# Performance work log

Measured on AMD Instinct MI355X. Metric: run time of the kernel, lower is better.

Reference implementation:

```python
import jax, jax.numpy as jnp
import numpy as np
from jax import lax

D_MODEL, D_STATE, D_CONV, EXPAND = 1024, 16, 4, 2
D_INNER = D_MODEL * EXPAND
LN_EPS = 1e-5


def _silu(v):
    return v * jax.nn.sigmoid(v)


def setup_inputs() -> dict:
    key = jax.random.key(0)
    ks = jax.random.split(key, 12)
    B, T = 4, 2048
    x = jax.random.normal(ks[0], (B, T, D_MODEL), dtype=jnp.float32)
    W_in = jax.random.normal(ks[1], (2 * D_INNER, D_MODEL), dtype=jnp.float32) * (D_MODEL ** -0.5)
    conv_w = jax.random.normal(ks[2], (D_INNER, 1, D_CONV), dtype=jnp.float32) * (D_CONV ** -0.5)
    conv_b = jax.random.normal(ks[3], (D_INNER,), dtype=jnp.float32) * 0.01
    W_x = jax.random.normal(ks[4], (2 * D_STATE, D_INNER), dtype=jnp.float32) * (D_INNER ** -0.5)
    dt_init_std = D_INNER ** -0.5
    W_dt = jax.random.uniform(ks[5], (D_INNER, D_INNER), minval=-dt_init_std, maxval=dt_init_std, dtype=jnp.float32)
    # bias = inverse softplus of dt sampled log-uniform in [dt_min, dt_max]
    dt = jnp.exp(jax.random.uniform(ks[6], (D_INNER,)) * (np.log(0.1) - np.log(0.001)) + np.log(0.001))
    b_dt = dt + jnp.log(-jnp.expm1(-dt))
    A_log = jnp.log(jnp.arange(1, D_STATE + 1, dtype=jnp.float32) * 0.5)
    D_param = jnp.ones((D_INNER,), dtype=jnp.float32)
    W_out = jax.random.normal(ks[7], (D_MODEL, D_INNER), dtype=jnp.float32) * (D_MODEL ** -0.5)
    ln_g = jnp.ones((D_INNER,), dtype=jnp.float32)
    ln_b = jnp.zeros((D_INNER,), dtype=jnp.float32)
    return {"x": x, "W_in": W_in, "conv_w": conv_w, "conv_b": conv_b, "W_x": W_x,
            "W_dt": W_dt, "b_dt": b_dt, "A_log": A_log, "D_param": D_param,
            "W_out": W_out, "ln_g": ln_g, "ln_b": ln_b}


def _forward(x, W_in, conv_w, conv_b, W_x, W_dt, b_dt, A_log, D_param, W_out, ln_g, ln_b):
    B, T, _ = x.shape
    xz = jnp.einsum('btd,ed->bte', x, W_in)            # (B,T,2*d_inner)
    xp, z = xz[..., :D_INNER], xz[..., D_INNER:]
    # depthwise causal conv1d (left pad d_conv-1, keep first T outputs)
    xc = lax.conv_general_dilated(
        jnp.transpose(xp, (0, 2, 1)), conv_w,
        window_strides=(1,), padding=[(D_CONV - 1, 0)],
        feature_group_count=D_INNER,
        dimension_numbers=('NCH', 'OIH', 'NCH')) + conv_b[None, :, None]
    xc = _silu(jnp.transpose(xc, (0, 2, 1)))           # (B,T,d_inner)
    ssm = jnp.einsum('bti,si->bts', xc, W_x)           # (B,T,2*d_state)
    Bp, Cp = ssm[..., :D_STATE], ssm[..., D_STATE:]
    dt = jax.nn.softplus(jnp.einsum('bti,oi->bto', xc, W_dt) + b_dt)
    A = -jnp.exp(A_log)                                # (d_state,)

    def step(h, inp):
        x_t, b_t, c_t, dt_t = inp                      # (B,d),(B,s),(B,s),(B,d)
        dA = jnp.exp(dt_t[..., None] * A)              # (B,d_inner,d_state)
        h = dA * h + (dt_t[..., None] * b_t[:, None, :]) * x_t[..., None]
        y_t = jnp.einsum('bds,bs->bd', h, c_t)
        return h, y_t

    h0 = jnp.zeros((B, D_INNER, D_STATE), dtype=x.dtype)
    tm = lambda a: jnp.moveaxis(a, 1, 0)               # time-major
    _, ys = lax.scan(step, h0, (tm(xc), tm(Bp), tm(Cp), tm(dt)))
    y = jnp.moveaxis(ys, 0, 1)                         # (B,T,d_inner)

    mu = jnp.mean(y, axis=-1, keepdims=True)
    var = jnp.mean((y - mu) ** 2, axis=-1, keepdims=True)
    y = (y - mu) * lax.rsqrt(var + LN_EPS) * ln_g + ln_b
    y = y + xc * D_param
    y = y * _silu(z)
    return jnp.einsum('bti,di->btd', y, W_out)         # dropout is identity (eval)


def reference(x, W_in, conv_w, conv_b, W_x, W_dt, b_dt, A_log, D_param, W_out, ln_g, ln_b):
    return _forward(x, W_in, conv_w, conv_b, W_x, W_dt, b_dt, A_log, D_param, W_out, ln_g, ln_b)
```

## Files before the change

kernel.cpp:

```cpp
#include <hip/hip_runtime.h>
#include <hip/hip_bf16.h>
#include <math.h>
#include <stdint.h>

#define B_SZ 4
#define T_SZ 2048
#define DM   1024
#define DI   2048
#define DS   16
#define BT   (B_SZ*T_SZ)
#define NC   2176

typedef __attribute__((ext_vector_type(8))) short short8;
typedef __attribute__((ext_vector_type(4))) float f32x4;

__device__ __forceinline__ float siluf(float v) { return v / (1.f + __expf(-v)); }
__device__ __forceinline__ float softplusf(float x) {
    return fmaxf(x, 0.f) + log1pf(__expf(-fabsf(x)));
}
__device__ __forceinline__ unsigned short f2b(float f) {
    __hip_bfloat16 h = __float2bfloat16(f);
    return *reinterpret_cast<unsigned short*>(&h);
}
__device__ __forceinline__ float b2f(unsigned short u) {
    unsigned v = (unsigned)u << 16;
    float f;
    __builtin_memcpy(&f, &v, 4);
    return f;
}
__device__ __forceinline__ void gld_lds16(const void* g, void* l) {
    __builtin_amdgcn_global_load_lds(
        (const __attribute__((address_space(1))) unsigned int*)g,
        (__attribute__((address_space(3))) unsigned int*)l,
        16, 0, 0);
}

__global__ __launch_bounds__(256)
void cvt_bf16(const float* __restrict__ src, unsigned short* __restrict__ dst, int n4)
{
    int i = blockIdx.x * 256 + threadIdx.x;
    if (i >= n4) return;
    float4 v = ((const float4*)src)[i];
    ushort4 o;
    o.x = f2b(v.x); o.y = f2b(v.y); o.z = f2b(v.z); o.w = f2b(v.w);
    ((ushort4*)dst)[i] = o;
}

__global__ __launch_bounds__(256)
void cvt_wc(const float* __restrict__ Wdt, const float* __restrict__ Wx,
            unsigned short* __restrict__ dst)
{
    const int n4 = NC * (DI / 4);
    int i = blockIdx.x * 256 + threadIdx.x;
    if (i >= n4) return;
    int row = i >> 9;
    int c4  = i & 511;
    float4 v;
    if (row < 2048)      v = ((const float4*)Wdt)[(size_t)row * 512 + c4];
    else if (row < 2080) v = ((const float4*)Wx)[(size_t)(row - 2048) * 512 + c4];
    else                 v = make_float4(0.f, 0.f, 0.f, 0.f);
    ushort4 o;
    o.x = f2b(v.x); o.y = f2b(v.y); o.z = f2b(v.z); o.w = f2b(v.w);
    ((ushort4*)dst)[i] = o;
}

__global__ __launch_bounds__(512)
void gemm_mfma(const unsigned short* __restrict__ A,
               const unsigned short* __restrict__ Bm,
               int M, int N, int K, int mode,
               const float* __restrict__ bias,
               void* __restrict__ o0, void* __restrict__ o1, void* __restrict__ o2)
{
    __shared__ unsigned short As[2][128 * 32];
    __shared__ unsigned short Bs[2][128 * 32];

    const int npn = N >> 7;
    const int pid = blockIdx.x;
    const int gsz = 16 * npn;
    const int gid = pid / gsz;
    const int pm  = gid * 16 + (pid % 16);
    const int pn  = (pid % gsz) / 16;
    const int bm  = pm * 128;
    const int bn  = pn * 128;

    const int tid  = threadIdx.x;
    const int lane = tid & 63;
    const int wave = tid >> 6;
    const int wm   = (wave >> 2) * 64;
    const int wn   = (wave & 3) * 32;

    f32x4 zero4 = {0.f, 0.f, 0.f, 0.f};
    f32x4 acc[4][2];
#pragma unroll
    for (int i = 0; i < 4; i++)
#pragma unroll
        for (int j = 0; j < 2; j++) acc[i][j] = zero4;

    const int sr    = tid >> 2;
    const int sgran = (tid & 3) ^ ((tid >> 3) & 3);
    const unsigned short* Ag = A  + (size_t)(bm + sr) * K + sgran * 8;
    const unsigned short* Bg = Bm + (size_t)(bn + sr) * K + sgran * 8;

    const int fr = lane & 15;
    const int fg = lane >> 4;
    int aoff[4], boff[2];
#pragma unroll
    for (int i = 0; i < 4; i++) {
        const int l = (wm + i * 16 + fr) * 64 + fg * 16;
        aoff[i] = l ^ (((l >> 7) & 3) << 4);
    }
#pragma unroll
    for (int j = 0; j < 2; j++) {
        const int l = (wn + j * 16 + fr) * 64 + fg * 16;
        boff[j] = l ^ (((l >> 7) & 3) << 4);
    }

    gld_lds16(Ag, &As[0][tid * 8]);
    gld_lds16(Bg, &Bs[0][tid * 8]);
    __syncthreads();

    int cur = 0;
    for (int k0 = 0; k0 < K; k0 += 32) {
        if (k0 + 32 < K) {
            gld_lds16(Ag + k0 + 32, &As[cur ^ 1][tid * 8]);
            gld_lds16(Bg + k0 + 32, &Bs[cur ^ 1][tid * 8]);
        }
        const char* Ab = (const char*)&As[cur][0];
        const char* Bb = (const char*)&Bs[cur][0];
        short8 af[4], bf[2];
#pragma unroll
        for (int i = 0; i < 4; i++)
            af[i] = *(const short8*)(Ab + aoff[i]);
#pragma unroll
        for (int j = 0; j < 2; j++)
            bf[j] = *(const short8*)(Bb + boff[j]);
#pragma unroll
        for (int i = 0; i < 4; i++)
#pragma unroll
            for (int j = 0; j < 2; j++)
                acc[i][j] = __builtin_amdgcn_mfma_f32_16x16x32_bf16(
                    af[i], bf[j], acc[i][j], 0, 0, 0);
        __syncthreads();
        cur ^= 1;
    }

    const int cr0 = bm + wm + (lane >> 4) * 4;
    const int cc0 = bn + wn + (lane & 15);
#pragma unroll
    for (int i = 0; i < 4; i++) {
#pragma unroll
        for (int j = 0; j < 2; j++) {
            const int col = cc0 + j * 16;
#pragma unroll
            for (int r = 0; r < 4; r++) {
                const int row = cr0 + i * 16 + r;
                float v = acc[i][j][r];
                if (mode == 0) {
                    if (col < 2048)
                        ((unsigned short*)o0)[(size_t)row * 2048 + col] = f2b(v);
                    else
                        ((unsigned short*)o1)[(size_t)row * 2048 + col - 2048] = f2b(v);
                } else if (mode == 1) {
                    if (col < 2048) {
                        ((float*)o0)[(size_t)row * 2048 + col] = softplusf(v + bias[col]);
                    } else if (col < 2064) {
                        ((float*)o1)[(size_t)row * DS + (col - 2048)] = v;
                    } else if (col < 2080) {
                        ((float*)o2)[(size_t)row * DS + (col - 2064)] = v;
                    }
                } else {
                    ((float*)o0)[(size_t)row * N + col] = v;
                }
            }
        }
    }
}

__global__ __launch_bounds__(256)
void conv_silu(const unsigned short* __restrict__ xpb, const float* __restrict__ cw,
               const float* __restrict__ cb, unsigned short* __restrict__ xcb)
{
    const int idx = blockIdx.x * 256 + threadIdx.x;
    const int i  = idx & (DI - 1);
    const int bt = idx >> 11;
    const int t  = bt & (T_SZ - 1);
    float acc = cb[i];
    float4 w = *(const float4*)(cw + (size_t)i * 4);
    float wr[4] = {w.x, w.y, w.z, w.w};
#pragma unroll
    for (int k = 0; k < 4; k++) {
        const int tt = t - 3 + k;
        if (tt >= 0)
            acc = fmaf(b2f(xpb[(size_t)(bt - 3 + k) * DI + i]), wr[k], acc);
    }
    xcb[idx] = f2b(siluf(acc));
}

#define CH 16
#define CL (T_SZ / CH)

__global__ __launch_bounds__(256)
void scan2(const unsigned short* __restrict__ xcb, float* __restrict__ dty,
           const float* __restrict__ Bp, const float* __restrict__ Cp,
           const float* __restrict__ A_log)
{
    __shared__ float shH[CH][16][DS];
    __shared__ float shP[CH][16][DS];
    __shared__ float shI[CH][16][DS];
    const int tid = threadIdx.x;
    const int c = tid >> 4;
    const int g = tid & 15;
    const int b = blockIdx.y;
    const int d = blockIdx.x * 16 + g;

    float A[DS];
#pragma unroll
    for (int s = 0; s < DS; s++) A[s] = -__expf(A_log[s]);

    const size_t colbase = (size_t)b * T_SZ * DI + d;
    const unsigned short* xp = xcb + colbase + (size_t)c * CL * DI;
    float* dp = dty + colbase + (size_t)c * CL * DI;
    const float4* Bb = (const float4*)(Bp + ((size_t)b * T_SZ + c * CL) * DS);
    const float4* Cb = (const float4*)(Cp + ((size_t)b * T_SZ + c * CL) * DS);

    float h[DS], P[DS];
#pragma unroll
    for (int s = 0; s < DS; s++) { h[s] = 0.f; P[s] = 1.f; }

    for (int i = 0; i < CL; i++) {
        const float xv = b2f(xp[(size_t)i * DI]);
        const float dv = dp[(size_t)i * DI];
        float4 Bv[4] = {Bb[i*4+0], Bb[i*4+1], Bb[i*4+2], Bb[i*4+3]};
        const float* bs = (const float*)&Bv[0];
        const float dx = dv * xv;
#pragma unroll
        for (int s = 0; s < DS; s++) {
            const float dA = __expf(dv * A[s]);
            h[s] = fmaf(dA, h[s], dx * bs[s]);
            P[s] *= dA;
        }
    }
#pragma unroll
    for (int s = 0; s < DS; s += 4) {
        *(float4*)&shH[c][g][s] = make_float4(h[s], h[s+1], h[s+2], h[s+3]);
        *(float4*)&shP[c][g][s] = make_float4(P[s], P[s+1], P[s+2], P[s+3]);
    }
    __syncthreads();

    {
        const int g2 = tid >> 4, s2 = tid & 15;
        float hin = 0.f;
        shI[0][g2][s2] = 0.f;
        for (int cc = 1; cc < CH; cc++) {
            hin = fmaf(shP[cc-1][g2][s2], hin, shH[cc-1][g2][s2]);
            shI[cc][g2][s2] = hin;
        }
    }
    __syncthreads();

#pragma unroll
    for (int s = 0; s < DS; s++) h[s] = shI[c][g][s];
    for (int i = 0; i < CL; i++) {
        const float xv = b2f(xp[(size_t)i * DI]);
        const float dv = dp[(size_t)i * DI];
        float4 Bv[4] = {Bb[i*4+0], Bb[i*4+1], Bb[i*4+2], Bb[i*4+3]};
        float4 Cv[4] = {Cb[i*4+0], Cb[i*4+1], Cb[i*4+2], Cb[i*4+3]};
        const float* bs = (const float*)&Bv[0];
        const float* cs = (const float*)&Cv[0];
        const float dx = dv * xv;
        float yv = 0.f;
#pragma unroll
        for (int s = 0; s < DS; s++) {
            const float dA = __expf(dv * A[s]);
            h[s] = fmaf(dA, h[s], dx * bs[s]);
            yv = fmaf(h[s], cs[s], yv);
        }
        dp[(size_t)i * DI] = yv;
    }
}

__global__ __launch_bounds__(256)
void ln_fuse(const float* __restrict__ y, const unsigned short* __restrict__ xcb,
             const unsigned short* __restrict__ zb, const float* __restrict__ g,
             const float* __restrict__ bln, const float* __restrict__ Dp,
             unsigned short* __restrict__ yb)
{
    __shared__ float rs[256], rss[256];
    const int bt  = blockIdx.x;
    const int tid = threadIdx.x;
    const float* yr = y + (size_t)bt * DI;
    const unsigned short* xr = xcb + (size_t)bt * DI;
    const unsigned short* zr = zb + (size_t)bt * DI;
    unsigned short* orow = yb + (size_t)bt * DI;

    float v[8];
    float s = 0.f, ss = 0.f;
#pragma unroll
    for (int j = 0; j < 8; j++) {
        v[j] = yr[tid + j * 256];
        s  += v[j];
        ss += v[j] * v[j];
    }
    rs[tid] = s; rss[tid] = ss;
    __syncthreads();
    for (int off = 128; off > 0; off >>= 1) {
        if (tid < off) { rs[tid] += rs[tid + off]; rss[tid] += rss[tid + off]; }
        __syncthreads();
    }
    const float mu   = rs[0] * (1.f / DI);
    const float var  = rss[0] * (1.f / DI) - mu * mu;
    const float rstd = rsqrtf(var + 1e-5f);
#pragma unroll
    for (int j = 0; j < 8; j++) {
        const int dcol = tid + j * 256;
        float yn = (v[j] - mu) * rstd * g[dcol] + bln[dcol];
        yn += b2f(xr[dcol]) * Dp[dcol];
        yn *= siluf(b2f(zr[dcol]));
        orow[dcol] = f2b(yn);
    }
}

extern "C" void kernel_launch(void* const* d_in, const int* in_sizes, int n_in,
                              void* d_out, int out_size, void* d_ws, size_t ws_size,
                              hipStream_t stream)
{
    const float* x      = (const float*)d_in[0];
    const float* W_in   = (const float*)d_in[1];
    const float* conv_w = (const float*)d_in[2];
    const float* conv_b = (const float*)d_in[3];
    const float* W_x    = (const float*)d_in[4];
    const float* W_dt   = (const float*)d_in[5];
    const float* b_dt   = (const float*)d_in[6];
    const float* A_log  = (const float*)d_in[7];
    const float* D_par  = (const float*)d_in[8];
    const float* W_out  = (const float*)d_in[9];
    const float* ln_g   = (const float*)d_in[10];
    const float* ln_b   = (const float*)d_in[11];
    float* out = (float*)d_out;

    char* w = (char*)d_ws;
    const size_t MB = 1ull << 20;
    unsigned short* xpb    = (unsigned short*)(w);
    unsigned short* zb     = (unsigned short*)(w + 32 * MB);
    unsigned short* xcb    = (unsigned short*)(w + 64 * MB);
    float*          dts    = (float*)(w + 96 * MB);
    unsigned short* xb     = (unsigned short*)(w + 96 * MB);
    unsigned short* W_inb  = (unsigned short*)(w + 112 * MB);
    unsigned short* Wcb    = (unsigned short*)(w + 160 * MB);
    unsigned short* W_outb = (unsigned short*)(w + 169 * MB);
    float*          BpF    = (float*)(w + 174 * MB);
    float*          CpF    = BpF + (size_t)BT * DS;
    unsigned short* yb     = xpb;

    dim3 blk(256);
    dim3 blk512(512);

    cvt_bf16<<<dim3((BT * DM / 4 + 255) / 256), blk, 0, stream>>>(x, xb, BT * DM / 4);
    cvt_bf16<<<dim3((2 * DI * DM / 4 + 255) / 256), blk, 0, stream>>>(W_in, W_inb, 2 * DI * DM / 4);
    cvt_wc<<<dim3((NC * DI / 4 + 255) / 256), blk, 0, stream>>>(W_dt, W_x, Wcb);
    cvt_bf16<<<dim3((DM * DI / 4 + 255) / 256), blk, 0, stream>>>(W_out, W_outb, DM * DI / 4);

    gemm_mfma<<<dim3((BT / 128) * (2 * DI / 128)), blk512, 0, stream>>>(
        xb, W_inb, BT, 2 * DI, DM, 0, nullptr, xpb, zb, nullptr);

    conv_silu<<<dim3(BT * DI / 256), blk, 0, stream>>>(xpb, conv_w, conv_b, xcb);

    gemm_mfma<<<dim3((BT / 128) * (NC / 128)), blk512, 0, stream>>>(
        xcb, Wcb, BT, NC, DI, 1, b_dt, dts, BpF, CpF);

    scan2<<<dim3(DI / 16, B_SZ), blk, 0, stream>>>(xcb, dts, BpF, CpF, A_log);

    ln_fuse<<<dim3(BT), blk, 0, stream>>>(dts, xcb, zb, ln_g, ln_b, D_par, yb);

    gemm_mfma<<<dim3((BT / 128) * (DM / 128)), blk512, 0, stream>>>(
        yb, W_outb, BT, DM, DI, 2, nullptr, out, nullptr, nullptr);
}
```

Baseline: 631.1 us.

## Restructure MFMA GEMM to 256 threads with 64x64 warp tiles and triple-buffered LDS

The GEMM kernel now runs 256 threads per block instead of 512, and each wave computes a 64x64 output tile instead of 64x32, which roughly halves LDS fragment reads per MFMA. Each thread issues two global-to-LDS loads per operand per stage. The K loop moves from double to triple buffering: it prefetches two stages ahead, uses explicit vmcnt waits with raw barriers, and raises wave priority around the MFMA block. In exchange it adds accumulator register pressure, uses more LDS per block, and depends on hand-written waitcnt correctness.

```diff
diff --git a/kernel.cpp b/kernel.cpp
--- a/kernel.cpp
+++ b/kernel.cpp
@@ -64,15 +64,15 @@
     ((ushort4*)dst)[i] = o;
 }
 
-__global__ __launch_bounds__(512)
+__global__ __launch_bounds__(256, 3)
 void gemm_mfma(const unsigned short* __restrict__ A,
                const unsigned short* __restrict__ Bm,
                int M, int N, int K, int mode,
                const float* __restrict__ bias,
                void* __restrict__ o0, void* __restrict__ o1, void* __restrict__ o2)
 {
-    __shared__ unsigned short As[2][128 * 32];
-    __shared__ unsigned short Bs[2][128 * 32];
+    __shared__ unsigned short As[3][128 * 32];
+    __shared__ unsigned short Bs[3][128 * 32];
 
     const int npn = N >> 7;
     const int pid = blockIdx.x;
@@ -86,75 +86,98 @@
     const int tid  = threadIdx.x;
     const int lane = tid & 63;
     const int wave = tid >> 6;
-    const int wm   = (wave >> 2) * 64;
-    const int wn   = (wave & 3) * 32;
+    const int wm   = (wave >> 1) * 64;
+    const int wn   = (wave & 1) * 64;
 
     f32x4 zero4 = {0.f, 0.f, 0.f, 0.f};
-    f32x4 acc[4][2];
+    f32x4 acc[4][4];
 #pragma unroll
     for (int i = 0; i < 4; i++)
 #pragma unroll
-        for (int j = 0; j < 2; j++) acc[i][j] = zero4;
+        for (int j = 0; j < 4; j++) acc[i][j] = zero4;
 
     const int sr    = tid >> 2;
     const int sgran = (tid & 3) ^ ((tid >> 3) & 3);
     const unsigned short* Ag = A  + (size_t)(bm + sr) * K + sgran * 8;
     const unsigned short* Bg = Bm + (size_t)(bn + sr) * K + sgran * 8;
+    const size_t rowK64 = (size_t)64 * K;
 
     const int fr = lane & 15;
     const int fg = lane >> 4;
-    int aoff[4], boff[2];
+    int aoff[4], boff[4];
 #pragma unroll
     for (int i = 0; i < 4; i++) {
         const int l = (wm + i * 16 + fr) * 64 + fg * 16;
         aoff[i] = l ^ (((l >> 7) & 3) << 4);
     }
 #pragma unroll
-    for (int j = 0; j < 2; j++) {
+    for (int j = 0; j < 4; j++) {
         const int l = (wn + j * 16 + fr) * 64 + fg * 16;
         boff[j] = l ^ (((l >> 7) & 3) << 4);
     }
 
-    gld_lds16(Ag, &As[0][tid * 8]);
-    gld_lds16(Bg, &Bs[0][tid * 8]);
-    __syncthreads();
-
-    int cur = 0;
-    for (int k0 = 0; k0 < K; k0 += 32) {
-        if (k0 + 32 < K) {
-            gld_lds16(Ag + k0 + 32, &As[cur ^ 1][tid * 8]);
-            gld_lds16(Bg + k0 + 32, &Bs[cur ^ 1][tid * 8]);
-        }
-        const char* Ab = (const char*)&As[cur][0];
-        const char* Bb = (const char*)&Bs[cur][0];
-        short8 af[4], bf[2];
+    const int NT = K >> 5;
+
+#define STAGE(b, t) do {                                          \
+        const size_t k0_ = (size_t)(t) * 32;                      \
+        gld_lds16(Ag + k0_,          &As[(b)][tid * 8]);          \
+        gld_lds16(Ag + rowK64 + k0_, &As[(b)][2048 + tid * 8]);   \
+        gld_lds16(Bg + k0_,          &Bs[(b)][tid * 8]);          \
+        gld_lds16(Bg + rowK64 + k0_, &Bs[(b)][2048 + tid * 8]);   \
+    } while (0)
+
+    STAGE(0, 0);
+    if (NT > 1) STAGE(1, 1);
+    asm volatile("s_waitcnt vmcnt(4)" ::: "memory");
+    __builtin_amdgcn_s_barrier();
+    asm volatile("" ::: "memory");
+
+    int r = 0, r2 = 2;
+    for (int t = 0; t < NT; ++t) {
+        const char* Ab = (const char*)&As[r][0];
+        const char* Bb = (const char*)&Bs[r][0];
+        short8 af[4], bf[4];
 #pragma unroll
         for (int i = 0; i < 4; i++)
             af[i] = *(const short8*)(Ab + aoff[i]);
 #pragma unroll
-        for (int j = 0; j < 2; j++)
+        for (int j = 0; j < 4; j++)
             bf[j] = *(const short8*)(Bb + boff[j]);
+
+        if (t + 2 < NT) STAGE(r2, t + 2);
+
+        __builtin_amdgcn_s_setprio(1);
 #pragma unroll
         for (int i = 0; i < 4; i++)
 #pragma unroll
-            for (int j = 0; j < 2; j++)
+            for (int j = 0; j < 4; j++)
                 acc[i][j] = __builtin_amdgcn_mfma_f32_16x16x32_bf16(
                     af[i], bf[j], acc[i][j], 0, 0, 0);
-        __syncthreads();
-        cur ^= 1;
-    }
-
-    const int cr0 = bm + wm + (lane >> 4) * 4;
-    const int cc0 = bn + wn + (lane & 15);
+        __builtin_amdgcn_s_setprio(0);
+
+        if (t + 1 < NT) {
+            if (t + 2 < NT) asm volatile("s_waitcnt vmcnt(4)" ::: "memory");
+            else            asm volatile("s_waitcnt vmcnt(0)" ::: "memory");
+            asm volatile("s_waitcnt lgkmcnt(0)" ::: "memory");
+            __builtin_amdgcn_s_barrier();
+            asm volatile("" ::: "memory");
+        }
+        r  = (r  == 2) ? 0 : r + 1;
+        r2 = (r2 == 2) ? 0 : r2 + 1;
+    }
+#undef STAGE
+
+    const int cr0 = bm + wm + fg * 4;
+    const int cc0 = bn + wn + fr;
 #pragma unroll
     for (int i = 0; i < 4; i++) {
 #pragma unroll
-        for (int j = 0; j < 2; j++) {
+        for (int j = 0; j < 4; j++) {
             const int col = cc0 + j * 16;
 #pragma unroll
-            for (int r = 0; r < 4; r++) {
-                const int row = cr0 + i * 16 + r;
-                float v = acc[i][j][r];
+            for (int rr = 0; rr < 4; rr++) {
+                const int row = cr0 + i * 16 + rr;
+                float v = acc[i][j][rr];
                 if (mode == 0) {
                     if (col < 2048)
                         ((unsigned short*)o0)[(size_t)row * 2048 + col] = f2b(v);
@@ -353,25 +376,24 @@
     unsigned short* yb     = xpb;
 
     dim3 blk(256);
-    dim3 blk512(512);
 
     cvt_bf16<<<dim3((BT * DM / 4 + 255) / 256), blk, 0, stream>>>(x, xb, BT * DM / 4);
     cvt_bf16<<<dim3((2 * DI * DM / 4 + 255) / 256), blk, 0, stream>>>(W_in, W_inb, 2 * DI * DM / 4);
     cvt_wc<<<dim3((NC * DI / 4 + 255) / 256), blk, 0, stream>>>(W_dt, W_x, Wcb);
     cvt_bf16<<<dim3((DM * DI / 4 + 255) / 256), blk, 0, stream>>>(W_out, W_outb, DM * DI / 4);
 
-    gemm_mfma<<<dim3((BT / 128) * (2 * DI / 128)), blk512, 0, stream>>>(
+    gemm_mfma<<<dim3((BT / 128) * (2 * DI / 128)), blk, 0, stream>>>(
         xb, W_inb, BT, 2 * DI, DM, 0, nullptr, xpb, zb, nullptr);
 
     conv_silu<<<dim3(BT * DI / 256), blk, 0, stream>>>(xpb, conv_w, conv_b, xcb);
 
-    gemm_mfma<<<dim3((BT / 128) * (NC / 128)), blk512, 0, stream>>>(
+    gemm_mfma<<<dim3((BT / 128) * (NC / 128)), blk, 0, stream>>>(
         xcb, Wcb, BT, NC, DI, 1, b_dt, dts, BpF, CpF);
 
     scan2<<<dim3(DI / 16, B_SZ), blk, 0, stream>>>(xcb, dts, BpF, CpF, A_log);
 
     ln_fuse<<<dim3(BT), blk, 0, stream>>>(dts, xcb, zb, ln_g, ln_b, D_par, yb);
 
-    gemm_mfma<<<dim3((BT / 128) * (DM / 128)), blk512, 0, stream>>>(
+    gemm_mfma<<<dim3((BT / 128) * (DM / 128)), blk, 0, stream>>>(
         yb, W_outb, BT, DM, DI, 2, nullptr, out, nullptr, nullptr);
 }
```

New measurement: 705.4 us. +11.8%, slower.
